# Kernel optimization log

Hardware: AMD Instinct MI355X
Metric: run time of the kernel (lower is better)

Reference implementation:

```python
import jax, jax.numpy as jnp
import numpy as np

EPS = 1e-12  # F.normalize default eps

def _l2norm(x):
    return x / jnp.maximum(jnp.linalg.norm(x, axis=-1, keepdims=True), EPS)

def setup_inputs() -> dict:
    key = jax.random.key(0)
    k1, k2, k3 = jax.random.split(key, 3)
    N, C, D = 131072, 1000, 256
    feat = jax.random.normal(k1, (N, D), dtype=jnp.float32)
    # memory bank is initialized to L2-normalized centers in the original (init())
    memory = _l2norm(jax.random.normal(k2, (C, D), dtype=jnp.float32))
    label = jax.random.randint(k3, (N,), 0, C, dtype=jnp.int64)
    return {"feat": feat, "memory": memory, "label": label}

def reference(feat, memory, label):
    num_cls, feat_dim = memory.shape
    N = feat.shape[0]
    t = 1.0  # forward default temperature

    featn = _l2norm(feat)

    # --- update(feat, label): fused per-class masked gather+sum as one segment_sum ---
    f = jax.lax.stop_gradient(featn)  # feat.detach() in original
    sums = jax.ops.segment_sum(f, label, num_segments=num_cls)          # [C, D]
    counts = jax.ops.segment_sum(jnp.ones((N,), f.dtype), label, num_segments=num_cls)
    flags = (counts > 0).astype(f.dtype)[:, None]                        # [C, 1]
    batch_center = _l2norm(sums) * flags                                 # zeros for empty classes

    # --- update_center_by_simi ---
    simi = jnp.sum(memory * batch_center, axis=-1, keepdims=True)        # [C, 1]
    update_wei = 1.0 - (1.0 - simi) * flags                              # [C, 1]
    new_memory = _l2norm(update_wei * memory + (1.0 - update_wei) * batch_center)

    # --- similarity + cross entropy ---
    simis = jnp.einsum('nd,cd->nc', featn, new_memory) / t               # [N, C]
    logp = jax.nn.log_softmax(simis, axis=-1)
    loss = -jnp.mean(jnp.take_along_axis(logp, label[:, None], axis=1))
    return loss
```

## Files before the change

kernel.cpp:

```cpp
#include <hip/hip_runtime.h>
#include <hip/hip_fp8.h>

#define NROWS 131072
#define NCLS  1000
#define CPAD  1024
#define DDIM  256

typedef __attribute__((ext_vector_type(4))) float f32x4;
typedef __attribute__((ext_vector_type(2))) long l64x2;

__device__ __forceinline__ float wred(float v){
#pragma unroll
  for (int m = 1; m < 64; m <<= 1) v += __shfl_xor(v, m, 64);
  return v;
}

__device__ __forceinline__ float fexp2(float x){
#if __has_builtin(__builtin_amdgcn_exp2f)
  return __builtin_amdgcn_exp2f(x);
#else
  float r; asm("v_exp_f32 %0, %1" : "=v"(r) : "v"(x)); return r;
#endif
}

__device__ __forceinline__ unsigned pk4_fp8(float a, float b, float c, float d){
#if __has_builtin(__builtin_amdgcn_cvt_pk_fp8_f32)
  int v = __builtin_amdgcn_cvt_pk_fp8_f32(a, b, 0, false);
  v = __builtin_amdgcn_cvt_pk_fp8_f32(c, d, v, true);
  return (unsigned)v;
#else
  __hip_fp8_e4m3 fa(a), fb(b), fc(c), fd(d);
  return (unsigned)fa.__x | ((unsigned)fb.__x<<8) |
         ((unsigned)fc.__x<<16) | ((unsigned)fd.__x<<24);
#endif
}

__device__ __forceinline__ void store_frag8(unsigned char* nmem, int c, int ln,
                                            float a, float b, float x, float y){
  int ch = c >> 5, nb = (c >> 4) & 1, r16 = c & 15;
  int k = ln >> 3, g = (ln >> 1) & 3, q = ln & 1;
  *(unsigned*)(nmem + ch*8192 + k*1024 + (g*16+r16)*16 + nb*8 + q*4) =
      pk4_fp8(a, b, x, y);
}

__global__ __launch_bounds__(1024) void k_center(
    const float* __restrict__ feat, const float* __restrict__ memory,
    const int* __restrict__ label, unsigned char* __restrict__ nmem){
  const int c0 = blockIdx.x * 2;
  const int t = threadIdx.x;
  const int w = t >> 6, lane = t & 63;
  if (c0 >= NCLS){
    if (t < 128) store_frag8(nmem, c0 + (t >> 6), t & 63, 0.f, 0.f, 0.f, 0.f);
    return;
  }
  const int c1 = c0 + 1;
  __shared__ float4 accred[2][16][64];
  __shared__ int cw[2][16];

  float4 a0 = make_float4(0.f,0.f,0.f,0.f);
  float4 a1 = make_float4(0.f,0.f,0.f,0.f);
  int cnt0 = 0, cnt1 = 0;
  const float4* feat4 = (const float4*)feat;
  const int4*   lab4  = (const int4*)label;

  for (int it = 0; it < 32; ++it){
    int base = (w*32 + it) * 256;
    int4 lv = lab4[base/4 + lane];
#pragma unroll
    for (int sub = 0; sub < 4; ++sub){
      int lvv = (sub==0)?lv.x:(sub==1)?lv.y:(sub==2)?lv.z:lv.w;
      unsigned long long m0 = __ballot(lvv == c0);
      unsigned long long m1 = __ballot(lvv == c1);
      cnt0 += (int)__popcll(m0); cnt1 += (int)__popcll(m1);
      while (m0){
        int b = __ffsll((long long)m0) - 1; m0 &= m0 - 1;
        int r = base + b*4 + sub;
        float4 x = feat4[r*64 + lane];
        float ss = wred(x.x*x.x + x.y*x.y + x.z*x.z + x.w*x.w);
        float sc = 1.0f / fmaxf(sqrtf(ss), 1e-12f);
        a0.x += x.x*sc; a0.y += x.y*sc; a0.z += x.z*sc; a0.w += x.w*sc;
      }
      while (m1){
        int b = __ffsll((long long)m1) - 1; m1 &= m1 - 1;
        int r = base + b*4 + sub;
        float4 x = feat4[r*64 + lane];
        float ss = wred(x.x*x.x + x.y*x.y + x.z*x.z + x.w*x.w);
        float sc = 1.0f / fmaxf(sqrtf(ss), 1e-12f);
        a1.x += x.x*sc; a1.y += x.y*sc; a1.z += x.z*sc; a1.w += x.w*sc;
      }
    }
  }
  accred[0][w][lane] = a0; accred[1][w][lane] = a1;
  if (lane == 0){ cw[0][w] = cnt0; cw[1][w] = cnt1; }
  __syncthreads();

  if (t < 128){
    int cls = t >> 6, ln = t & 63;
    float sx=0.f, sy=0.f, sz=0.f, sw=0.f; int total = 0;
#pragma unroll
    for (int s = 0; s < 16; ++s){
      float4 v = accred[cls][s][ln];
      sx += v.x; sy += v.y; sz += v.z; sw += v.w;
      total += cw[cls][s];
    }
    int c = c0 + cls;
    float ss = wred(sx*sx + sy*sy + sz*sz + sw*sw);
    float inv = 1.0f / fmaxf(sqrtf(ss), 1e-12f);
    float bx = sx*inv, by = sy*inv, bz = sz*inv, bw = sw*inv;
    float flag = (total > 0) ? 1.0f : 0.0f;
    float4 m = ((const float4*)memory)[c*64 + ln];
    float simi = wred(m.x*bx + m.y*by + m.z*bz + m.w*bw);
    float wei = 1.0f - (1.0f - simi)*flag;
    float rx = wei*m.x + (1.0f-wei)*bx;
    float ry = wei*m.y + (1.0f-wei)*by;
    float rz = wei*m.z + (1.0f-wei)*bz;
    float rw = wei*m.w + (1.0f-wei)*bw;
    float ss2 = wred(rx*rx + ry*ry + rz*rz + rw*rw);
    float inv2 = 1.0f / fmaxf(sqrtf(ss2), 1e-12f);
    store_frag8(nmem, c, ln, rx*inv2, ry*inv2, rz*inv2, rw*inv2);
  }
}

#define MFMA8 __builtin_amdgcn_mfma_f32_16x16x32_fp8_fp8

__global__ __launch_bounds__(256, 2) void k_gemm(
    const float* __restrict__ feat, const unsigned char* __restrict__ nmem,
    const int* __restrict__ label, float* __restrict__ partials){
  __shared__ float bred[4];
  const int t = threadIdx.x, w = t >> 6, lane = t & 63;
  const int g = lane >> 4, r16 = lane & 15;
  const int rowbase = blockIdx.x * 128;

  long areg[2][8];
  float rs_self[2];
#pragma unroll
  for (int mf = 0; mf < 2; ++mf){
    int row = rowbase + w*32 + mf*16 + r16;
    const float4* rp = (const float4*)(feat + row*DDIM);
    float ss = 0.f;
#pragma unroll
    for (int kt = 0; kt < 8; ++kt){
      float4 x0 = rp[kt*8 + g*2];
      float4 x1 = rp[kt*8 + g*2 + 1];
      ss += x0.x*x0.x + x0.y*x0.y + x0.z*x0.z + x0.w*x0.w
          + x1.x*x1.x + x1.y*x1.y + x1.z*x1.z + x1.w*x1.w;
      unsigned lo = pk4_fp8(x0.x, x0.y, x0.z, x0.w);
      unsigned hi = pk4_fp8(x1.x, x1.y, x1.z, x1.w);
      areg[mf][kt] = (long)(((unsigned long)hi << 32) | lo);
    }
    ss += __shfl_xor(ss, 16, 64);
    ss += __shfl_xor(ss, 32, 64);
    rs_self[mf] = 1.0f / fmaxf(sqrtf(ss), 1e-12f);
  }

  int labreg[2][4];
  float rs2[2][4];
#pragma unroll
  for (int m = 0; m < 2; ++m)
#pragma unroll
    for (int j = 0; j < 4; ++j){
      int rr = w*32 + m*16 + g*4 + j;
      labreg[m][j] = label[rowbase + rr];
      rs2[m][j] = __shfl(rs_self[m], g*4 + j, 16) * 1.44269504f;
    }

  float esum[2][4] = {{0.f,0.f,0.f,0.f},{0.f,0.f,0.f,0.f}};
  float slb [2][4] = {{0.f,0.f,0.f,0.f},{0.f,0.f,0.f,0.f}};

  const char* nbp = (const char*)nmem + lane*16;
  const int rot = blockIdx.x & 31;
  long bA[8], bB[8];

#define LOADLO(CH)                                                            \
  { const char* cb = nbp + (size_t)(CH)*8192;                                 \
    _Pragma("unroll")                                                         \
    for (int k2 = 0; k2 < 4; ++k2){                                           \
      l64x2 v = *(const l64x2*)(cb + k2*1024);                                \
      bA[k2*2] = v.x; bA[k2*2+1] = v.y; } }
#define LOADHI(CH)                                                            \
  { const char* cb = nbp + (size_t)(CH)*8192 + 4096;                          \
    _Pragma("unroll")                                                         \
    for (int k2 = 0; k2 < 4; ++k2){                                           \
      l64x2 v = *(const l64x2*)(cb + k2*1024);                                \
      bB[k2*2] = v.x; bB[k2*2+1] = v.y; } }

  LOADLO(rot); LOADHI(rot);

  for (int it = 0; it < 32; ++it){
    int cur = (it + rot) & 31;
    int nxt = (it + 1 + rot) & 31;

    f32x4 acc[2][2];
    __builtin_amdgcn_s_setprio(1);
    {
      f32x4 Z = {0.f,0.f,0.f,0.f};
      acc[0][0] = MFMA8(areg[0][0], bA[0], Z, 0, 0, 0);
      acc[0][1] = MFMA8(areg[0][0], bA[1], Z, 0, 0, 0);
      acc[1][0] = MFMA8(areg[1][0], bA[0], Z, 0, 0, 0);
      acc[1][1] = MFMA8(areg[1][0], bA[1], Z, 0, 0, 0);
    }
#pragma unroll
    for (int k = 1; k < 4; ++k){
      acc[0][0] = MFMA8(areg[0][k], bA[k*2+0], acc[0][0], 0, 0, 0);
      acc[0][1] = MFMA8(areg[0][k], bA[k*2+1], acc[0][1], 0, 0, 0);
      acc[1][0] = MFMA8(areg[1][k], bA[k*2+0], acc[1][0], 0, 0, 0);
      acc[1][1] = MFMA8(areg[1][k], bA[k*2+1], acc[1][1], 0, 0, 0);
    }
    __builtin_amdgcn_s_setprio(0);

    if (it < 31) LOADLO(nxt);

    __builtin_amdgcn_s_setprio(1);
#pragma unroll
    for (int k = 4; k < 8; ++k){
      acc[0][0] = MFMA8(areg[0][k], bB[(k-4)*2+0], acc[0][0], 0, 0, 0);
      acc[0][1] = MFMA8(areg[0][k], bB[(k-4)*2+1], acc[0][1], 0, 0, 0);
      acc[1][0] = MFMA8(areg[1][k], bB[(k-4)*2+0], acc[1][0], 0, 0, 0);
      acc[1][1] = MFMA8(areg[1][k], bB[(k-4)*2+1], acc[1][1], 0, 0, 0);
    }
    __builtin_amdgcn_s_setprio(0);

    if (it < 31) LOADHI(nxt);

#pragma unroll
    for (int m = 0; m < 2; ++m)
#pragma unroll
      for (int n = 0; n < 2; ++n){
        int col = cur*32 + n*16 + r16;
#pragma unroll
        for (int j = 0; j < 4; ++j){
          float v = acc[m][n][j] * rs2[m][j];
          esum[m][j] += fexp2(v);
          slb[m][j] = (col == labreg[m][j]) ? v : slb[m][j];
        }
      }
  }

  float v = 0.f;
#pragma unroll
  for (int m = 0; m < 2; ++m)
#pragma unroll
    for (int j = 0; j < 4; ++j){
      float e = esum[m][j], s = slb[m][j];
      e += __shfl_xor(e, 1, 64); e += __shfl_xor(e, 2, 64);
      e += __shfl_xor(e, 4, 64); e += __shfl_xor(e, 8, 64);
      s += __shfl_xor(s, 1, 64); s += __shfl_xor(s, 2, 64);
      s += __shfl_xor(s, 4, 64); s += __shfl_xor(s, 8, 64);
      v += 0.69314718056f * (__log2f(e - 24.0f) - s);
    }
  if (r16 != 0) v = 0.f;
  v = wred(v);
  if (lane == 0) bred[w] = v;
  __syncthreads();
  if (t == 0) partials[blockIdx.x] = bred[0] + bred[1] + bred[2] + bred[3];
}

__global__ __launch_bounds__(256) void k_final(
    const float* __restrict__ partials, float* __restrict__ out){
  const int t = threadIdx.x;
  const int w = t >> 6, lane = t & 63;
  __shared__ float red[4];
  float s = partials[t] + partials[t+256] + partials[t+512] + partials[t+768];
  s = wred(s);
  if (lane == 0) red[w] = s;
  __syncthreads();
  if (t == 0) out[0] = (red[0]+red[1]+red[2]+red[3]) * (1.0f/(float)NROWS);
}

extern "C" void kernel_launch(void* const* d_in, const int* in_sizes, int n_in,
                              void* d_out, int out_size, void* d_ws, size_t ws_size,
                              hipStream_t stream){
  const float* feat   = (const float*)d_in[0];
  const float* memory = (const float*)d_in[1];
  const int*   label  = (const int*)d_in[2];
  float* out = (float*)d_out;
  unsigned char* nmem = (unsigned char*)d_ws;
  float* partials = (float*)((char*)d_ws + 524288);

  k_center<<<CPAD/2, 1024, 0, stream>>>(feat, memory, label, nmem);
  k_gemm<<<NROWS/128, 256, 0, stream>>>(feat, nmem, label, partials);
  k_final<<<1, 256, 0, stream>>>(partials, out);
}
```

Before: 111.6 us.

## Double rows per wave in fused GEMM-softmax to reuse memory-bank fragments

Each wave now handles 64 rows (four 16-row MFMA fragments) instead of 32, so every B fragment loaded from the FP8 memory bank feeds twice as many MFMAs. The grid halves to 512 blocks and the final reduction sums 512 partials. This cuts B-operand global/L2 traffic per row and raises MFMA density per load. In exchange, register pressure roughly doubles for A registers and accumulators, which can threaten the 2-blocks-per-CU occupancy, and fewer blocks means less latency hiding across the 256 CUs.

```diff
diff --git a/kernel.cpp b/kernel.cpp
--- a/kernel.cpp
+++ b/kernel.cpp
@@ -129,13 +129,13 @@
   __shared__ float bred[4];
   const int t = threadIdx.x, w = t >> 6, lane = t & 63;
   const int g = lane >> 4, r16 = lane & 15;
-  const int rowbase = blockIdx.x * 128;
-
-  long areg[2][8];
-  float rs_self[2];
-#pragma unroll
-  for (int mf = 0; mf < 2; ++mf){
-    int row = rowbase + w*32 + mf*16 + r16;
+  const int rowbase = blockIdx.x * 256;
+
+  long areg[4][8];
+  float rs_self[4];
+#pragma unroll
+  for (int mf = 0; mf < 4; ++mf){
+    int row = rowbase + w*64 + mf*16 + r16;
     const float4* rp = (const float4*)(feat + row*DDIM);
     float ss = 0.f;
 #pragma unroll
@@ -153,19 +153,22 @@
     rs_self[mf] = 1.0f / fmaxf(sqrtf(ss), 1e-12f);
   }
 
-  int labreg[2][4];
-  float rs2[2][4];
-#pragma unroll
-  for (int m = 0; m < 2; ++m)
+  int labreg[4][4];
+  float rs2[4][4];
+#pragma unroll
+  for (int m = 0; m < 4; ++m)
 #pragma unroll
     for (int j = 0; j < 4; ++j){
-      int rr = w*32 + m*16 + g*4 + j;
+      int rr = w*64 + m*16 + g*4 + j;
       labreg[m][j] = label[rowbase + rr];
       rs2[m][j] = __shfl(rs_self[m], g*4 + j, 16) * 1.44269504f;
     }
 
-  float esum[2][4] = {{0.f,0.f,0.f,0.f},{0.f,0.f,0.f,0.f}};
-  float slb [2][4] = {{0.f,0.f,0.f,0.f},{0.f,0.f,0.f,0.f}};
+  float esum[4][4], slb[4][4];
+#pragma unroll
+  for (int m = 0; m < 4; ++m)
+#pragma unroll
+    for (int j = 0; j < 4; ++j){ esum[m][j] = 0.f; slb[m][j] = 0.f; }
 
   const char* nbp = (const char*)nmem + lane*16;
   const int rot = blockIdx.x & 31;
@@ -190,40 +193,41 @@
     int cur = (it + rot) & 31;
     int nxt = (it + 1 + rot) & 31;
 
-    f32x4 acc[2][2];
+    f32x4 acc[4][2];
     __builtin_amdgcn_s_setprio(1);
     {
       f32x4 Z = {0.f,0.f,0.f,0.f};
-      acc[0][0] = MFMA8(areg[0][0], bA[0], Z, 0, 0, 0);
-      acc[0][1] = MFMA8(areg[0][0], bA[1], Z, 0, 0, 0);
-      acc[1][0] = MFMA8(areg[1][0], bA[0], Z, 0, 0, 0);
-      acc[1][1] = MFMA8(areg[1][0], bA[1], Z, 0, 0, 0);
-    }
-#pragma unroll
-    for (int k = 1; k < 4; ++k){
-      acc[0][0] = MFMA8(areg[0][k], bA[k*2+0], acc[0][0], 0, 0, 0);
-      acc[0][1] = MFMA8(areg[0][k], bA[k*2+1], acc[0][1], 0, 0, 0);
-      acc[1][0] = MFMA8(areg[1][k], bA[k*2+0], acc[1][0], 0, 0, 0);
-      acc[1][1] = MFMA8(areg[1][k], bA[k*2+1], acc[1][1], 0, 0, 0);
-    }
+#pragma unroll
+      for (int m = 0; m < 4; ++m){
+        acc[m][0] = MFMA8(areg[m][0], bA[0], Z, 0, 0, 0);
+        acc[m][1] = MFMA8(areg[m][0], bA[1], Z, 0, 0, 0);
+      }
+    }
+#pragma unroll
+    for (int k = 1; k < 4; ++k)
+#pragma unroll
+      for (int m = 0; m < 4; ++m){
+        acc[m][0] = MFMA8(areg[m][k], bA[k*2+0], acc[m][0], 0, 0, 0);
+        acc[m][1] = MFMA8(areg[m][k], bA[k*2+1], acc[m][1], 0, 0, 0);
+      }
     __builtin_amdgcn_s_setprio(0);
 
     if (it < 31) LOADLO(nxt);
 
     __builtin_amdgcn_s_setprio(1);
 #pragma unroll
-    for (int k = 4; k < 8; ++k){
-      acc[0][0] = MFMA8(areg[0][k], bB[(k-4)*2+0], acc[0][0], 0, 0, 0);
-      acc[0][1] = MFMA8(areg[0][k], bB[(k-4)*2+1], acc[0][1], 0, 0, 0);
-      acc[1][0] = MFMA8(areg[1][k], bB[(k-4)*2+0], acc[1][0], 0, 0, 0);
-      acc[1][1] = MFMA8(areg[1][k], bB[(k-4)*2+1], acc[1][1], 0, 0, 0);
-    }
+    for (int k = 4; k < 8; ++k)
+#pragma unroll
+      for (int m = 0; m < 4; ++m){
+        acc[m][0] = MFMA8(areg[m][k], bB[(k-4)*2+0], acc[m][0], 0, 0, 0);
+        acc[m][1] = MFMA8(areg[m][k], bB[(k-4)*2+1], acc[m][1], 0, 0, 0);
+      }
     __builtin_amdgcn_s_setprio(0);
 
     if (it < 31) LOADHI(nxt);
 
 #pragma unroll
-    for (int m = 0; m < 2; ++m)
+    for (int m = 0; m < 4; ++m)
 #pragma unroll
       for (int n = 0; n < 2; ++n){
         int col = cur*32 + n*16 + r16;
@@ -238,7 +242,7 @@
 
   float v = 0.f;
 #pragma unroll
-  for (int m = 0; m < 2; ++m)
+  for (int m = 0; m < 4; ++m)
 #pragma unroll
     for (int j = 0; j < 4; ++j){
       float e = esum[m][j], s = slb[m][j];
@@ -260,7 +264,7 @@
   const int t = threadIdx.x;
   const int w = t >> 6, lane = t & 63;
   __shared__ float red[4];
-  float s = partials[t] + partials[t+256] + partials[t+512] + partials[t+768];
+  float s = partials[t] + partials[t+256];
   s = wred(s);
   if (lane == 0) red[w] = s;
   __syncthreads();
@@ -278,6 +282,6 @@
   float* partials = (float*)((char*)d_ws + 524288);
 
   k_center<<<CPAD/2, 1024, 0, stream>>>(feat, memory, label, nmem);
-  k_gemm<<<NROWS/128, 256, 0, stream>>>(feat, nmem, label, partials);
+  k_gemm<<<NROWS/256, 256, 0, stream>>>(feat, nmem, label, partials);
   k_final<<<1, 256, 0, stream>>>(partials, out);
 }
```

Measured after the change: 115.1 us. 1.03x slower.

## Compute label logit directly in fp32 and pre-scale A operand

Applied to the files above, without the earlier changes.

k_center now also writes the normalized memory rows as fp32. k_gemm computes each row's target logit as a direct fp32 dot product with its label's center, replacing the per-tile column-compare select and its shuffle reduction. The row's 1/norm·log2e scale is folded into the fp8 quantization of feat, so the epilogue only takes exp2 of the accumulators. The cost is re-reading feat rows plus a gathered 1KB center row per row, and it changes fp8 quantization range and accuracy because of the prescaling.

```diff
diff --git a/kernel.cpp b/kernel.cpp
--- a/kernel.cpp
+++ b/kernel.cpp
@@ -45,7 +45,8 @@
 
 __global__ __launch_bounds__(1024) void k_center(
     const float* __restrict__ feat, const float* __restrict__ memory,
-    const int* __restrict__ label, unsigned char* __restrict__ nmem){
+    const int* __restrict__ label, unsigned char* __restrict__ nmem,
+    float* __restrict__ nmemf32){
   const int c0 = blockIdx.x * 2;
   const int t = threadIdx.x;
   const int w = t >> 6, lane = t & 63;
@@ -118,6 +119,8 @@
     float ss2 = wred(rx*rx + ry*ry + rz*rz + rw*rw);
     float inv2 = 1.0f / fmaxf(sqrtf(ss2), 1e-12f);
     store_frag8(nmem, c, ln, rx*inv2, ry*inv2, rz*inv2, rw*inv2);
+    ((float4*)nmemf32)[c*64 + ln] =
+        make_float4(rx*inv2, ry*inv2, rz*inv2, rw*inv2);
   }
 }
 
@@ -125,14 +128,15 @@
 
 __global__ __launch_bounds__(256, 2) void k_gemm(
     const float* __restrict__ feat, const unsigned char* __restrict__ nmem,
-    const int* __restrict__ label, float* __restrict__ partials){
+    const float* __restrict__ nmemf32, const int* __restrict__ label,
+    float* __restrict__ partials){
   __shared__ float bred[4];
   const int t = threadIdx.x, w = t >> 6, lane = t & 63;
   const int g = lane >> 4, r16 = lane & 15;
   const int rowbase = blockIdx.x * 128;
 
   long areg[2][8];
-  float rs_self[2];
+  float slabv[2];
 #pragma unroll
   for (int mf = 0; mf < 2; ++mf){
     int row = rowbase + w*32 + mf*16 + r16;
@@ -144,28 +148,38 @@
       float4 x1 = rp[kt*8 + g*2 + 1];
       ss += x0.x*x0.x + x0.y*x0.y + x0.z*x0.z + x0.w*x0.w
           + x1.x*x1.x + x1.y*x1.y + x1.z*x1.z + x1.w*x1.w;
-      unsigned lo = pk4_fp8(x0.x, x0.y, x0.z, x0.w);
-      unsigned hi = pk4_fp8(x1.x, x1.y, x1.z, x1.w);
-      areg[mf][kt] = (long)(((unsigned long)hi << 32) | lo);
     }
     ss += __shfl_xor(ss, 16, 64);
     ss += __shfl_xor(ss, 32, 64);
-    rs_self[mf] = 1.0f / fmaxf(sqrtf(ss), 1e-12f);
-  }
-
-  int labreg[2][4];
-  float rs2[2][4];
+    float invn = 1.0f / fmaxf(sqrtf(ss), 1e-12f);
+    float sc = 1.44269504f * invn;
+    int lab = label[row];
+    const float4* bp4 = (const float4*)(nmemf32 + (size_t)lab*DDIM);
+    float dl = 0.f;
+#pragma unroll
+    for (int kt = 0; kt < 8; ++kt){
+      float4 x0 = rp[kt*8 + g*2];
+      float4 x1 = rp[kt*8 + g*2 + 1];
+      float4 b0 = bp4[kt*8 + g*2];
+      float4 b1 = bp4[kt*8 + g*2 + 1];
+      unsigned lo = pk4_fp8(x0.x*sc, x0.y*sc, x0.z*sc, x0.w*sc);
+      unsigned hi = pk4_fp8(x1.x*sc, x1.y*sc, x1.z*sc, x1.w*sc);
+      areg[mf][kt] = (long)(((unsigned long)hi << 32) | lo);
+      dl += x0.x*b0.x + x0.y*b0.y + x0.z*b0.z + x0.w*b0.w
+          + x1.x*b1.x + x1.y*b1.y + x1.z*b1.z + x1.w*b1.w;
+    }
+    dl += __shfl_xor(dl, 16, 64);
+    dl += __shfl_xor(dl, 32, 64);
+    slabv[mf] = dl * invn;
+  }
+  float slab_epi[2][4];
 #pragma unroll
   for (int m = 0; m < 2; ++m)
 #pragma unroll
-    for (int j = 0; j < 4; ++j){
-      int rr = w*32 + m*16 + g*4 + j;
-      labreg[m][j] = label[rowbase + rr];
-      rs2[m][j] = __shfl(rs_self[m], g*4 + j, 16) * 1.44269504f;
-    }
+    for (int j = 0; j < 4; ++j)
+      slab_epi[m][j] = __shfl(slabv[m], g*4 + j, 16);
 
   float esum[2][4] = {{0.f,0.f,0.f,0.f},{0.f,0.f,0.f,0.f}};
-  float slb [2][4] = {{0.f,0.f,0.f,0.f},{0.f,0.f,0.f,0.f}};
 
   const char* nbp = (const char*)nmem + lane*16;
   const int rot = blockIdx.x & 31;
@@ -187,7 +201,6 @@
   LOADLO(rot); LOADHI(rot);
 
   for (int it = 0; it < 32; ++it){
-    int cur = (it + rot) & 31;
     int nxt = (it + 1 + rot) & 31;
 
     f32x4 acc[2][2];
@@ -225,15 +238,10 @@
 #pragma unroll
     for (int m = 0; m < 2; ++m)
 #pragma unroll
-      for (int n = 0; n < 2; ++n){
-        int col = cur*32 + n*16 + r16;
-#pragma unroll
-        for (int j = 0; j < 4; ++j){
-          float v = acc[m][n][j] * rs2[m][j];
-          esum[m][j] += fexp2(v);
-          slb[m][j] = (col == labreg[m][j]) ? v : slb[m][j];
-        }
-      }
+      for (int n = 0; n < 2; ++n)
+#pragma unroll
+        for (int j = 0; j < 4; ++j)
+          esum[m][j] += fexp2(acc[m][n][j]);
   }
 
   float v = 0.f;
@@ -241,12 +249,10 @@
   for (int m = 0; m < 2; ++m)
 #pragma unroll
     for (int j = 0; j < 4; ++j){
-      float e = esum[m][j], s = slb[m][j];
+      float e = esum[m][j];
       e += __shfl_xor(e, 1, 64); e += __shfl_xor(e, 2, 64);
       e += __shfl_xor(e, 4, 64); e += __shfl_xor(e, 8, 64);
-      s += __shfl_xor(s, 1, 64); s += __shfl_xor(s, 2, 64);
-      s += __shfl_xor(s, 4, 64); s += __shfl_xor(s, 8, 64);
-      v += 0.69314718056f * (__log2f(e - 24.0f) - s);
+      v += 0.69314718056f * __log2f(e - 24.0f) - slab_epi[m][j];
     }
   if (r16 != 0) v = 0.f;
   v = wred(v);
@@ -275,9 +281,10 @@
   const int*   label  = (const int*)d_in[2];
   float* out = (float*)d_out;
   unsigned char* nmem = (unsigned char*)d_ws;
-  float* partials = (float*)((char*)d_ws + 524288);
-
-  k_center<<<CPAD/2, 1024, 0, stream>>>(feat, memory, label, nmem);
-  k_gemm<<<NROWS/128, 256, 0, stream>>>(feat, nmem, label, partials);
+  float* nmemf32 = (float*)((char*)d_ws + 262144);
+  float* partials = (float*)((char*)d_ws + 1310720);
+
+  k_center<<<CPAD/2, 1024, 0, stream>>>(feat, memory, label, nmem, nmemf32);
+  k_gemm<<<NROWS/128, 256, 0, stream>>>(feat, nmem, nmemf32, label, partials);
   k_final<<<1, 256, 0, stream>>>(partials, out);
 }
```

New measurement: 112.3 us. About the same (+0.6%).
